# Kernel optimization log

Measured on AMD Instinct MI355X. Metric: run time of the kernel, lower is better.

The kernel has to match this reference:

```python
import jax, jax.numpy as jnp
import numpy as np

D_K = 64
POS_WIN = 2.0

def setup_inputs() -> dict:
    key = jax.random.key(0)
    k1, k2, k3, k4 = jax.random.split(key, 4)
    B, H, S, D = 2, 8, 2048, D_K
    q = jax.random.normal(k1, (B, H, S, D), dtype=jnp.float32)
    k = jax.random.normal(k2, (B, H, S, D), dtype=jnp.float32)
    v = jax.random.normal(k3, (B, H, S, D), dtype=jnp.float32)
    # graph positional distances; module turns them into a Gaussian bias
    graph_attn_bias = jax.random.uniform(k4, (B, H, S, S), dtype=jnp.float32)
    return {"q": q, "k": k, "v": v, "graph_attn_bias": graph_attn_bias}

def reference(q, k, v, graph_attn_bias):
    # attn = (q / sqrt(d_k)) @ k^T  -> [B, H, Sq, Sk]
    scale = 1.0 / jnp.sqrt(jnp.float32(D_K))
    attn = jnp.einsum('bhqd,bhkd->bhqk', q * scale, k)
    # Gaussian positional bias: -0.5 * dist^2 / (0.5 * pos_win)^2
    gaussian_w = (-0.5 / (0.5 * POS_WIN) ** 2) * jnp.square(graph_attn_bias)
    attn = attn + gaussian_w
    weights = jax.nn.softmax(attn, axis=-1)  # dropout p=0.0 -> identity
    graph_out = jnp.einsum('bhqk,bhkd->bhqd', weights, v)
    return (graph_out, weights)
```

## Files before the change

kernel.cpp:

```cpp
#include <hip/hip_runtime.h>
#include <cstdint>

#define S 2048
#define D 64
#define QT 16
#define EPAD 8
#define ESTRIDE (S + EPAD)

typedef __attribute__((ext_vector_type(8))) short short8;
typedef __attribute__((ext_vector_type(4))) short short4v;
typedef __attribute__((ext_vector_type(4))) float floatx4;

static __device__ __forceinline__ unsigned short f2bf(float f) {
    union { float f; uint32_t u; } v; v.f = f;
    uint32_t r = (v.u + 0x7fffu + ((v.u >> 16) & 1u)) >> 16;
    return (unsigned short)r;
}
static __device__ __forceinline__ float bf2f(unsigned short s) {
    union { uint32_t u; float f; } v; v.u = ((uint32_t)s) << 16;
    return v.f;
}

__global__ void convert_bf16_kernel(const float* __restrict__ in,
                                    unsigned short* __restrict__ out, int n8) {
    int i = (blockIdx.x * 256 + threadIdx.x);
    if (i >= n8) return;
    const float* p = in + (size_t)i * 8;
    short8 o;
    #pragma unroll
    for (int j = 0; j < 8; ++j) o[j] = (short)f2bf(p[j]);
    *(short8*)(out + (size_t)i * 8) = o;
}

__global__ void transpose_v_kernel(const float* __restrict__ v,
                                   unsigned short* __restrict__ vt) {
    __shared__ unsigned short tile[64][72];
    const int tid = threadIdx.x;
    const int bh = blockIdx.x >> 5;
    const int s0 = (blockIdx.x & 31) * 64;
    #pragma unroll
    for (int rep = 0; rep < 16; ++rep) {
        int idx = rep * 256 + tid;
        int sl = idx >> 6, d = idx & 63;
        tile[sl][d] = f2bf(v[((size_t)bh * S + s0 + sl) * D + d]);
    }
    __syncthreads();
    #pragma unroll
    for (int rep = 0; rep < 16; ++rep) {
        int idx = rep * 256 + tid;
        int d = idx >> 6, sl = idx & 63;
        vt[((size_t)bh * D + d) * S + s0 + sl] = tile[sl][d];
    }
}

template <bool PRE>
__global__ __launch_bounds__(512, 4)
void attn_kernel(const float* __restrict__ q,
                 const float* __restrict__ k,
                 const float* __restrict__ v,
                 const float* __restrict__ bias,
                 const unsigned short* __restrict__ kb16,
                 const unsigned short* __restrict__ vt16,
                 float* __restrict__ gout,
                 float* __restrict__ wout)
{
    __shared__ __align__(16) unsigned short Elds[QT][ESTRIDE];
    __shared__ __align__(16) float pacc[QT][D];
    __shared__ float rowsum[QT];

    const int tid  = threadIdx.x;
    const int wv   = tid >> 6;
    const int lane = tid & 63;
    const int quad = lane >> 4;
    const int l16  = lane & 15;

    const int bh = blockIdx.x >> 7;
    const int qt = blockIdx.x & 127;
    const int q0 = qt * QT;

    if (tid < QT) rowsum[tid] = 0.0f;
    __syncthreads();

    short8 bq[2];
    {
        const float* qrow = q + ((size_t)bh * S + q0 + l16) * D;
        #pragma unroll
        for (int s = 0; s < 2; ++s) {
            const float* p = qrow + s * 32 + quad * 8;
            #pragma unroll
            for (int j = 0; j < 8; ++j) bq[s][j] = (short)f2bf(p[j]);
        }
    }

    const float* brow = bias + ((size_t)bh * S + q0 + l16) * S;

    float psum = 0.0f;
    for (int t = 0; t < 16; ++t) {
        const int kb = t * 128 + wv * 16;
        short8 ak[2];
        if (PRE) {
            const unsigned short* kr = kb16 + ((size_t)bh * S + kb + l16) * D;
            ak[0] = *(const short8*)(kr + quad * 8);
            ak[1] = *(const short8*)(kr + 32 + quad * 8);
        } else {
            const float* krow = k + ((size_t)bh * S + kb + l16) * D;
            #pragma unroll
            for (int s = 0; s < 2; ++s) {
                const float* p = krow + s * 32 + quad * 8;
                #pragma unroll
                for (int j = 0; j < 8; ++j) ak[s][j] = (short)f2bf(p[j]);
            }
        }
        floatx4 c = {0.f, 0.f, 0.f, 0.f};
        c = __builtin_amdgcn_mfma_f32_16x16x32_bf16(ak[0], bq[0], c, 0, 0, 0);
        c = __builtin_amdgcn_mfma_f32_16x16x32_bf16(ak[1], bq[1], c, 0, 0, 0);
        const floatx4 b4 = *(const floatx4*)(brow + kb + quad * 4);
        short4v ev;
        #pragma unroll
        for (int r = 0; r < 4; ++r) {
            const float logit = c[r] * 0.125f - 0.5f * b4[r] * b4[r];
            const float e = __expf(logit);
            psum += e;
            ev[r] = (short)f2bf(e);
        }
        *(short4v*)&Elds[l16][kb + quad * 4] = ev;
    }
    psum += __shfl_xor(psum, 16);
    psum += __shfl_xor(psum, 32);
    if (lane < 16) atomicAdd(&rowsum[l16], psum);

    __syncthreads();

    {
        const int r = tid >> 5;
        const int l = tid & 31;
        const float rinv = 1.0f / rowsum[r];
        float* wrow = wout + ((size_t)bh * S + q0 + r) * S;
        #pragma unroll 4
        for (int it = 0; it < 16; ++it) {
            const int col = it * 128 + l * 4;
            short4v evv = *(const short4v*)&Elds[r][col];
            floatx4 o;
            #pragma unroll
            for (int j = 0; j < 4; ++j) o[j] = bf2f((unsigned short)evv[j]) * rinv;
            *(floatx4*)(wrow + col) = o;
        }
    }

    {
        const int dt = wv & 3;
        const int kh = wv >> 2;
        const int dimc = dt * 16 + l16;
        floatx4 acc = {0.f, 0.f, 0.f, 0.f};
        if (PRE) {
            const unsigned short* vrow = vt16 + ((size_t)bh * D + dimc) * S + kh * 1024;
            const unsigned short* erow = &Elds[l16][kh * 1024];
            for (int sl = 0; sl < 32; ++sl) {
                const int sb = sl * 32 + quad * 8;
                short8 af  = *(const short8*)(erow + sb);
                short8 bfv = *(const short8*)(vrow + sb);
                acc = __builtin_amdgcn_mfma_f32_16x16x32_bf16(af, bfv, acc, 0, 0, 0);
            }
        } else {
            const float* vcol = v + (size_t)bh * S * D + dimc;
            for (int sl = 0; sl < 32; ++sl) {
                const int sb = kh * 1024 + sl * 32 + quad * 8;
                short8 af = *(const short8*)&Elds[l16][sb];
                short8 bfv;
                #pragma unroll
                for (int j = 0; j < 8; ++j)
                    bfv[j] = (short)f2bf(vcol[(size_t)(sb + j) * D]);
                acc = __builtin_amdgcn_mfma_f32_16x16x32_bf16(af, bfv, acc, 0, 0, 0);
            }
        }
        if (kh == 1) {
            #pragma unroll
            for (int r = 0; r < 4; ++r) pacc[quad * 4 + r][dimc] = acc[r];
        }
        __syncthreads();
        if (kh == 0) {
            #pragma unroll
            for (int r = 0; r < 4; ++r) {
                const int row = quad * 4 + r;
                const float rinv = 1.0f / rowsum[row];
                gout[((size_t)bh * S + q0 + row) * D + dimc] =
                    (acc[r] + pacc[row][dimc]) * rinv;
            }
        }
    }
}

extern "C" void kernel_launch(void* const* d_in, const int* in_sizes, int n_in,
                              void* d_out, int out_size, void* d_ws, size_t ws_size,
                              hipStream_t stream) {
    const float* q    = (const float*)d_in[0];
    const float* k    = (const float*)d_in[1];
    const float* v    = (const float*)d_in[2];
    const float* bias = (const float*)d_in[3];
    const int BH = in_sizes[0] / (S * D);
    float* gout = (float*)d_out;
    float* wout = gout + (size_t)BH * S * D;

    const size_t nkv = (size_t)BH * S * D;
    const bool pre = ws_size >= nkv * 2 * sizeof(unsigned short);

    dim3 grid(BH * (S / QT));

    if (pre) {
        unsigned short* kb16 = (unsigned short*)d_ws;
        unsigned short* vt16 = kb16 + nkv;
        int n8 = (int)(nkv / 8);
        convert_bf16_kernel<<<(n8 + 255) / 256, 256, 0, stream>>>(k, kb16, n8);
        transpose_v_kernel<<<BH * (S / 64), 256, 0, stream>>>(v, vt16);
        attn_kernel<true><<<grid, dim3(512), 0, stream>>>(q, k, v, bias, kb16, vt16, gout, wout);
    } else {
        attn_kernel<false><<<grid, dim3(512), 0, stream>>>(q, k, v, bias, nullptr, nullptr, gout, wout);
    }
}
```

Measured before the change: 539.3 us.

## Software-pipeline K/bias and V loads with register prefetch, widen weight stores

The QK loop keeps four iterations of K and bias loads in flight in registers, prefetching four steps ahead so MFMA and exp work overlap global memory latency. The PV loop also prefetches V four steps ahead and splits accumulation into two independent accumulators to shorten the MFMA dependency chain. The weights write-out now reads 8 bf16 values per LDS access and issues two float4 stores per iteration. Register pressure rises, which may hurt occupancy under the 512x4 launch bounds.

Result: no change. 543.6 us (+0.8%).

```diff
diff --git a/kernel.cpp b/kernel.cpp
--- a/kernel.cpp
+++ b/kernel.cpp
@@ -95,14 +95,56 @@
     const float* brow = bias + ((size_t)bh * S + q0 + l16) * S;
 
     float psum = 0.0f;
-    for (int t = 0; t < 16; ++t) {
-        const int kb = t * 128 + wv * 16;
-        short8 ak[2];
-        if (PRE) {
-            const unsigned short* kr = kb16 + ((size_t)bh * S + kb + l16) * D;
-            ak[0] = *(const short8*)(kr + quad * 8);
-            ak[1] = *(const short8*)(kr + 32 + quad * 8);
-        } else {
+    if (PRE) {
+        const unsigned short* kbase = kb16 + ((size_t)bh * S + l16) * D + quad * 8;
+        floatx4 bb[4];
+        short8 ak0[4], ak1[4];
+        #pragma unroll
+        for (int p = 0; p < 4; ++p) {
+            const int kb = p * 128 + wv * 16;
+            const unsigned short* kr = kbase + (size_t)kb * D;
+            ak0[p] = *(const short8*)kr;
+            ak1[p] = *(const short8*)(kr + 32);
+            bb[p]  = *(const floatx4*)(brow + kb + quad * 4);
+        }
+        #define QK_STEP(u, TT, PF) { \
+            const int kb_ = (TT) * 128 + wv * 16; \
+            floatx4 c = {0.f, 0.f, 0.f, 0.f}; \
+            c = __builtin_amdgcn_mfma_f32_16x16x32_bf16(ak0[u], bq[0], c, 0, 0, 0); \
+            c = __builtin_amdgcn_mfma_f32_16x16x32_bf16(ak1[u], bq[1], c, 0, 0, 0); \
+            const floatx4 bqd = bb[u]; \
+            if (PF) { \
+                const int kb2_ = kb_ + 512; \
+                const unsigned short* kr_ = kbase + (size_t)kb2_ * D; \
+                ak0[u] = *(const short8*)kr_; \
+                ak1[u] = *(const short8*)(kr_ + 32); \
+                bb[u]  = *(const floatx4*)(brow + kb2_ + quad * 4); \
+            } \
+            short4v ev; \
+            _Pragma("unroll") \
+            for (int r = 0; r < 4; ++r) { \
+                const float logit = c[r] * 0.125f - 0.5f * bqd[r] * bqd[r]; \
+                const float e = __expf(logit); \
+                psum += e; \
+                ev[r] = (short)f2bf(e); \
+            } \
+            *(short4v*)&Elds[l16][kb_ + quad * 4] = ev; \
+        }
+        for (int t = 0; t < 12; t += 4) {
+            QK_STEP(0, t + 0, 1)
+            QK_STEP(1, t + 1, 1)
+            QK_STEP(2, t + 2, 1)
+            QK_STEP(3, t + 3, 1)
+        }
+        QK_STEP(0, 12, 0)
+        QK_STEP(1, 13, 0)
+        QK_STEP(2, 14, 0)
+        QK_STEP(3, 15, 0)
+        #undef QK_STEP
+    } else {
+        for (int t = 0; t < 16; ++t) {
+            const int kb = t * 128 + wv * 16;
+            short8 ak[2];
             const float* krow = k + ((size_t)bh * S + kb + l16) * D;
             #pragma unroll
             for (int s = 0; s < 2; ++s) {
@@ -110,20 +152,20 @@
                 #pragma unroll
                 for (int j = 0; j < 8; ++j) ak[s][j] = (short)f2bf(p[j]);
             }
-        }
-        floatx4 c = {0.f, 0.f, 0.f, 0.f};
-        c = __builtin_amdgcn_mfma_f32_16x16x32_bf16(ak[0], bq[0], c, 0, 0, 0);
-        c = __builtin_amdgcn_mfma_f32_16x16x32_bf16(ak[1], bq[1], c, 0, 0, 0);
-        const floatx4 b4 = *(const floatx4*)(brow + kb + quad * 4);
-        short4v ev;
-        #pragma unroll
-        for (int r = 0; r < 4; ++r) {
-            const float logit = c[r] * 0.125f - 0.5f * b4[r] * b4[r];
-            const float e = __expf(logit);
-            psum += e;
-            ev[r] = (short)f2bf(e);
-        }
-        *(short4v*)&Elds[l16][kb + quad * 4] = ev;
+            floatx4 c = {0.f, 0.f, 0.f, 0.f};
+            c = __builtin_amdgcn_mfma_f32_16x16x32_bf16(ak[0], bq[0], c, 0, 0, 0);
+            c = __builtin_amdgcn_mfma_f32_16x16x32_bf16(ak[1], bq[1], c, 0, 0, 0);
+            const floatx4 b4 = *(const floatx4*)(brow + kb + quad * 4);
+            short4v ev;
+            #pragma unroll
+            for (int r = 0; r < 4; ++r) {
+                const float logit = c[r] * 0.125f - 0.5f * b4[r] * b4[r];
+                const float e = __expf(logit);
+                psum += e;
+                ev[r] = (short)f2bf(e);
+            }
+            *(short4v*)&Elds[l16][kb + quad * 4] = ev;
+        }
     }
     psum += __shfl_xor(psum, 16);
     psum += __shfl_xor(psum, 32);
@@ -136,14 +178,17 @@
         const int l = tid & 31;
         const float rinv = 1.0f / rowsum[r];
         float* wrow = wout + ((size_t)bh * S + q0 + r) * S;
-        #pragma unroll 4
-        for (int it = 0; it < 16; ++it) {
-            const int col = it * 128 + l * 4;
-            short4v evv = *(const short4v*)&Elds[r][col];
-            floatx4 o;
-            #pragma unroll
-            for (int j = 0; j < 4; ++j) o[j] = bf2f((unsigned short)evv[j]) * rinv;
-            *(floatx4*)(wrow + col) = o;
+        #pragma unroll 2
+        for (int it = 0; it < 8; ++it) {
+            const int col = it * 256 + l * 8;
+            short8 ev8 = *(const short8*)&Elds[r][col];
+            floatx4 o0, o1;
+            #pragma unroll
+            for (int j = 0; j < 4; ++j) o0[j] = bf2f((unsigned short)ev8[j]) * rinv;
+            #pragma unroll
+            for (int j = 0; j < 4; ++j) o1[j] = bf2f((unsigned short)ev8[j + 4]) * rinv;
+            *(floatx4*)(wrow + col) = o0;
+            *(floatx4*)(wrow + col + 4) = o1;
         }
     }
 
@@ -151,16 +196,31 @@
         const int dt = wv & 3;
         const int kh = wv >> 2;
         const int dimc = dt * 16 + l16;
-        floatx4 acc = {0.f, 0.f, 0.f, 0.f};
+        floatx4 acc0 = {0.f, 0.f, 0.f, 0.f};
+        floatx4 acc1 = {0.f, 0.f, 0.f, 0.f};
         if (PRE) {
-            const unsigned short* vrow = vt16 + ((size_t)bh * D + dimc) * S + kh * 1024;
-            const unsigned short* erow = &Elds[l16][kh * 1024];
-            for (int sl = 0; sl < 32; ++sl) {
-                const int sb = sl * 32 + quad * 8;
-                short8 af  = *(const short8*)(erow + sb);
-                short8 bfv = *(const short8*)(vrow + sb);
-                acc = __builtin_amdgcn_mfma_f32_16x16x32_bf16(af, bfv, acc, 0, 0, 0);
-            }
+            const unsigned short* vrow = vt16 + ((size_t)bh * D + dimc) * S
+                                       + kh * 1024 + quad * 8;
+            const unsigned short* erow = &Elds[l16][kh * 1024 + quad * 8];
+            short8 vv[4];
+            #pragma unroll
+            for (int p = 0; p < 4; ++p) vv[p] = *(const short8*)(vrow + p * 32);
+            #define PV_STEP(u, SL, PF, ACC) { \
+                short8 af = *(const short8*)(erow + (SL) * 32); \
+                ACC = __builtin_amdgcn_mfma_f32_16x16x32_bf16(af, vv[u], ACC, 0, 0, 0); \
+                if (PF) vv[u] = *(const short8*)(vrow + ((SL) + 4) * 32); \
+            }
+            for (int sl = 0; sl < 28; sl += 4) {
+                PV_STEP(0, sl + 0, 1, acc0)
+                PV_STEP(1, sl + 1, 1, acc1)
+                PV_STEP(2, sl + 2, 1, acc0)
+                PV_STEP(3, sl + 3, 1, acc1)
+            }
+            PV_STEP(0, 28, 0, acc0)
+            PV_STEP(1, 29, 0, acc1)
+            PV_STEP(2, 30, 0, acc0)
+            PV_STEP(3, 31, 0, acc1)
+            #undef PV_STEP
         } else {
             const float* vcol = v + (size_t)bh * S * D + dimc;
             for (int sl = 0; sl < 32; ++sl) {
@@ -170,9 +230,10 @@
                 #pragma unroll
                 for (int j = 0; j < 8; ++j)
                     bfv[j] = (short)f2bf(vcol[(size_t)(sb + j) * D]);
-                acc = __builtin_amdgcn_mfma_f32_16x16x32_bf16(af, bfv, acc, 0, 0, 0);
-            }
-        }
+                acc0 = __builtin_amdgcn_mfma_f32_16x16x32_bf16(af, bfv, acc0, 0, 0, 0);
+            }
+        }
+        floatx4 acc = acc0 + acc1;
         if (kh == 1) {
             #pragma unroll
             for (int r = 0; r < 4; ++r) pacc[quad * 4 + r][dimc] = acc[r];
```
